# Performance work log

Measured on AMD Instinct MI355X. Metric: run time of the kernel, lower is better.

## Reference

```python
import jax, jax.numpy as jnp
import numpy as np

EPS = 1e-5

def _layer_norm(x, gamma, beta):
    mu = jnp.mean(x, axis=-1, keepdims=True)
    var = jnp.var(x, axis=-1, keepdims=True)
    return (x - mu) * jax.lax.rsqrt(var + EPS) * gamma + beta

def setup_inputs() -> dict:
    key = jax.random.key(0)
    ks = jax.random.split(key, 4)
    B, T, D, H = 16, 2048, 1024, 1024
    s_in = 1.0 / np.sqrt(D)
    return {
        "x": jax.random.normal(ks[0], (B, T, D), dtype=jnp.float32),
        "c": jnp.zeros((B, H), dtype=jnp.float32),
        "W_lt": jax.random.uniform(ks[1], (H, D), jnp.float32, -s_in, s_in),
        "W_g": jax.random.uniform(ks[2], (2 * H, D), jnp.float32, -s_in, s_in),
        "b_g": jnp.zeros((2 * H,), dtype=jnp.float32),
        "gamma_g": jnp.ones((2 * H,), dtype=jnp.float32),
        "beta_g": jnp.zeros((2 * H,), dtype=jnp.float32),
        "gamma_a": jnp.ones((H,), dtype=jnp.float32),
        "beta_a": jnp.zeros((H,), dtype=jnp.float32),
    }

def reference(x, c, W_lt, W_g, b_g, gamma_g, beta_g, gamma_a, beta_a):
    H = W_lt.shape[0]
    # x: [B,T,D]
    x_tilde = jnp.einsum("btd,hd->bth", x, W_lt)            # [B,T,H]
    gate = jax.nn.sigmoid(_layer_norm(jnp.einsum("btd,gd->btg", x, W_g) + b_g, gamma_g, beta_g))
    f = gate[:, :, :H]                                        # forget gate [B,T,H]
    r = gate[:, :, H:]                                        # reset gate  [B,T,H]
    new_data = (1.0 - f) * x_tilde

    def step(c_prev, ft_nd):
        f_t, nd_t = ft_nd
        c_t = f_t * c_prev + nd_t
        return c_t, c_t

    # scan over time: move T to leading axis
    c_final, all_c = jax.lax.scan(step, c, (jnp.swapaxes(f, 0, 1), jnp.swapaxes(new_data, 0, 1)))
    all_c = jnp.swapaxes(all_c, 0, 1)                         # [B,T,H]
    h = r * jax.nn.sigmoid(_layer_norm(all_c, gamma_a, beta_a)) + (1.0 - r) * x
    return (h, c_final)
```

## Files before the change

kernel.cpp:

```cpp
#include <hip/hip_runtime.h>
#include <stdint.h>

typedef unsigned short u16;
typedef u16 us8 __attribute__((ext_vector_type(8)));
typedef uint32_t u32x8 __attribute__((ext_vector_type(8)));
typedef __bf16 bf16x8 __attribute__((ext_vector_type(8)));
typedef float f32x4 __attribute__((ext_vector_type(4)));

#define BB 16
#define TT 2048
#define HH 1024
#define MM 32768
#define NN 3072
#define KK 1024

__device__ __forceinline__ float b2f(u16 u) {
    union { uint32_t i; float f; } v; v.i = ((uint32_t)u) << 16; return v.f;
}
__device__ __forceinline__ u16 f2b(float f) {
    union { uint32_t i; float f; } v; v.f = f;
    uint32_t r = v.i + 0x7fffu + ((v.i >> 16) & 1u);
    return (u16)(r >> 16);
}
__device__ __forceinline__ float sigm(float z) {
    return 1.f / (1.f + __expf(-z));
}
__device__ __forceinline__ void load_lds16(const u16* g, u16* l) {
    __builtin_amdgcn_global_load_lds(
        (const __attribute__((address_space(1))) void*)g,
        (__attribute__((address_space(3))) void*)l, 16, 0, 0);
}

__global__ __launch_bounds__(256) void k_cvt(const float* __restrict__ x,
                                             const float* __restrict__ wlt,
                                             const float* __restrict__ wg,
                                             u16* __restrict__ xb,
                                             u16* __restrict__ wb) {
    long i = (long)(blockIdx.x * 256 + threadIdx.x) * 8;
    const float* s;
    u16* o;
    if (i < 33554432L) { s = x + i; o = xb + i; }
    else {
        long j = i - 33554432L;
        s = (j < 1048576L) ? (wlt + j) : (wg + (j - 1048576L));
        o = wb + j;
    }
    float4 a = *(const float4*)(s);
    float4 b = *(const float4*)(s + 4);
    us8 r;
    r[0] = f2b(a.x); r[1] = f2b(a.y); r[2] = f2b(a.z); r[3] = f2b(a.w);
    r[4] = f2b(b.x); r[5] = f2b(b.y); r[6] = f2b(b.z); r[7] = f2b(b.w);
    *(us8*)o = r;
}

__global__ __launch_bounds__(256) void k_gemm(const u16* __restrict__ A,
                                              const u16* __restrict__ W,
                                              u16* __restrict__ Y) {
    __shared__ u16 As[128 * 32];
    __shared__ u16 Bs[128 * 32];
    const int tid = threadIdx.x;
    const int lane = tid & 63;
    const int q = lane >> 4;
    const int l16 = lane & 15;
    const int w = tid >> 6;
    const int wm = (w >> 1) * 64, wn = (w & 1) * 64;
    const int bx = blockIdx.x, by = blockIdx.y;

    const int s0 = w * 128 + lane;
    const int s1 = w * 128 + 64 + lane;
    const u16* ag0 = A + (size_t)(by * 128 + (s0 >> 2)) * KK + (s0 & 3) * 8;
    const u16* ag1 = A + (size_t)(by * 128 + (s1 >> 2)) * KK + (s1 & 3) * 8;
    const u16* wg0 = W + (size_t)(bx * 128 + (s0 >> 2)) * KK + (s0 & 3) * 8;
    const u16* wg1 = W + (size_t)(bx * 128 + (s1 >> 2)) * KK + (s1 & 3) * 8;
    u16* al0 = As + w * 1024;
    u16* al1 = As + w * 1024 + 512;
    u16* bl0 = Bs + w * 1024;
    u16* bl1 = Bs + w * 1024 + 512;

    f32x4 zero = {0.f, 0.f, 0.f, 0.f};
    f32x4 acc[4][4];
#pragma unroll
    for (int i = 0; i < 4; i++)
#pragma unroll
        for (int j = 0; j < 4; j++) acc[i][j] = zero;

    for (int k0 = 0; k0 < KK; k0 += 32) {
        __syncthreads();
        load_lds16(ag0 + k0, al0);
        load_lds16(ag1 + k0, al1);
        load_lds16(wg0 + k0, bl0);
        load_lds16(wg1 + k0, bl1);
        __syncthreads();
        bf16x8 af[4], bv[4];
#pragma unroll
        for (int i = 0; i < 4; i++)
            af[i] = *(const bf16x8*)&As[(wm + i * 16 + l16) * 32 + q * 8];
#pragma unroll
        for (int j = 0; j < 4; j++)
            bv[j] = *(const bf16x8*)&Bs[(wn + j * 16 + l16) * 32 + q * 8];
#pragma unroll
        for (int i = 0; i < 4; i++)
#pragma unroll
            for (int j = 0; j < 4; j++)
                acc[i][j] = __builtin_amdgcn_mfma_f32_16x16x32_bf16(
                    af[i], bv[j], acc[i][j], 0, 0, 0);
    }

#pragma unroll
    for (int i = 0; i < 4; i++) {
#pragma unroll
        for (int rg = 0; rg < 4; rg++) {
            int row = by * 128 + wm + i * 16 + q * 4 + rg;
            u16* yp = Y + (size_t)row * NN + bx * 128 + wn + l16;
#pragma unroll
            for (int j = 0; j < 4; j++) yp[j * 16] = f2b(acc[i][j][rg]);
        }
    }
}

__global__ __launch_bounds__(256) void k_lnsig(const u16* __restrict__ Y,
                                               const float* __restrict__ bg,
                                               const float* __restrict__ gg,
                                               const float* __restrict__ bt,
                                               uint32_t* __restrict__ FN,
                                               u16* __restrict__ R) {
    const int row = blockIdx.x;
    const int t = threadIdx.x;
    const u16* yr = Y + (size_t)row * 3072;
    us8 gv = *(const us8*)(yr + 1024 + t * 8);
    float z[8];
    float s = 0.f, s2 = 0.f;
#pragma unroll
    for (int k = 0; k < 8; k++) {
        z[k] = b2f(gv[k]) + bg[t * 8 + k];
        s += z[k];
        s2 += z[k] * z[k];
    }
#pragma unroll
    for (int m = 1; m < 64; m <<= 1) {
        s += __shfl_xor(s, m);
        s2 += __shfl_xor(s2, m);
    }
    __shared__ float red[8];
    if ((t & 63) == 0) { red[t >> 6] = s; red[(t >> 6) + 4] = s2; }
    __syncthreads();
    s = red[0] + red[1] + red[2] + red[3];
    s2 = red[4] + red[5] + red[6] + red[7];
    const float mu = s * (1.f / 2048.f);
    const float inv = rsqrtf(s2 * (1.f / 2048.f) - mu * mu + 1e-5f);
    float gate[8];
#pragma unroll
    for (int k = 0; k < 8; k++)
        gate[k] = sigm((z[k] - mu) * inv * gg[t * 8 + k] + bt[t * 8 + k]);
    if (t < 128) {
        us8 xt = *(const us8*)(yr + t * 8);
        u32x8 fn;
#pragma unroll
        for (int k = 0; k < 8; k++) {
            u16 fb = f2b(gate[k]);
            u16 nb = f2b((1.f - gate[k]) * b2f(xt[k]));
            fn[k] = (uint32_t)fb | ((uint32_t)nb << 16);
        }
        *(u32x8*)(FN + (size_t)row * 1024 + t * 8) = fn;
    } else {
        us8 ro;
#pragma unroll
        for (int k = 0; k < 8; k++) ro[k] = f2b(gate[k]);
        *(us8*)(R + (size_t)row * 1024 + (t - 128) * 8) = ro;
    }
}

__global__ __launch_bounds__(256) void k_scan1(const uint32_t* __restrict__ FN,
                                               float2* __restrict__ agg) {
    int u = blockIdx.x * 256 + threadIdx.x;
    int h = u & 1023;
    int chunk = (u >> 10) & 31;
    int b = u >> 15;
    int base = (b * 2048 + chunk * 64) * 1024 + h;
    float Fp = 1.f, Np = 0.f;
#pragma unroll 4
    for (int i = 0; i < 64; i++) {
        uint32_t v = FN[base + i * 1024];
        float f = b2f((u16)(v & 0xffffu));
        float n = b2f((u16)(v >> 16));
        Np = fmaf(f, Np, n);
        Fp *= f;
    }
    agg[(b * 1024 + h) * 32 + chunk] = make_float2(Fp, Np);
}

__global__ __launch_bounds__(256) void k_scan2(const float2* __restrict__ agg,
                                               const float* __restrict__ c0,
                                               float* __restrict__ P) {
    int u = blockIdx.x * 256 + threadIdx.x;
    float c = c0[u];
    const float2* a = agg + (size_t)u * 32;
    float* p = P + (size_t)u * 32;
#pragma unroll 4
    for (int k = 0; k < 32; k++) {
        p[k] = c;
        float2 fn = a[k];
        c = fmaf(fn.x, c, fn.y);
    }
}

__global__ __launch_bounds__(256) void k_scan3(const uint32_t* __restrict__ FN,
                                               const float* __restrict__ P,
                                               u16* __restrict__ C,
                                               float* __restrict__ cfin) {
    int u = blockIdx.x * 256 + threadIdx.x;
    int h = u & 1023;
    int chunk = (u >> 10) & 31;
    int b = u >> 15;
    int base = (b * 2048 + chunk * 64) * 1024 + h;
    float c = P[(b * 1024 + h) * 32 + chunk];
#pragma unroll 4
    for (int i = 0; i < 64; i++) {
        uint32_t v = FN[base + i * 1024];
        float f = b2f((u16)(v & 0xffffu));
        float n = b2f((u16)(v >> 16));
        c = fmaf(f, c, n);
        C[base + i * 1024] = f2b(c);
    }
    if (chunk == 31) cfin[b * 1024 + h] = c;
}

__global__ __launch_bounds__(256) void k_final(const u16* __restrict__ C,
                                               const u16* __restrict__ R,
                                               const u16* __restrict__ xb,
                                               const float* __restrict__ ga,
                                               const float* __restrict__ ba,
                                               float* __restrict__ Ho) {
    const int w = threadIdx.x >> 6, lane = threadIdx.x & 63;
    const int row = blockIdx.x * 4 + w;
    const int col = lane * 16;
    const u16* cp = C + (size_t)row * 1024 + col;
    us8 cv0 = *(const us8*)cp;
    us8 cv1 = *(const us8*)(cp + 8);
    float c[16];
    float s = 0.f, s2 = 0.f;
#pragma unroll
    for (int k = 0; k < 8; k++) { c[k] = b2f(cv0[k]); c[8 + k] = b2f(cv1[k]); }
#pragma unroll
    for (int k = 0; k < 16; k++) { s += c[k]; s2 += c[k] * c[k]; }
#pragma unroll
    for (int m = 1; m < 64; m <<= 1) {
        s += __shfl_xor(s, m);
        s2 += __shfl_xor(s2, m);
    }
    const float mu = s * (1.f / 1024.f);
    const float inv = rsqrtf(s2 * (1.f / 1024.f) - mu * mu + 1e-5f);
    const u16* rp = R + (size_t)row * 1024 + col;
    us8 rv0 = *(const us8*)rp;
    us8 rv1 = *(const us8*)(rp + 8);
    const u16* xp = xb + (size_t)row * 1024 + col;
    us8 xv0 = *(const us8*)xp;
    us8 xv1 = *(const us8*)(xp + 8);
    float ho[16];
#pragma unroll
    for (int k = 0; k < 16; k++) {
        float sg = sigm((c[k] - mu) * inv * ga[col + k] + ba[col + k]);
        float rr = b2f(k < 8 ? rv0[k] : rv1[k - 8]);
        float xx = b2f(k < 8 ? xv0[k] : xv1[k - 8]);
        ho[k] = rr * sg + (1.f - rr) * xx;
    }
    float* op = Ho + (size_t)row * 1024 + col;
    *(float4*)(op)      = *(float4*)&ho[0];
    *(float4*)(op + 4)  = *(float4*)&ho[4];
    *(float4*)(op + 8)  = *(float4*)&ho[8];
    *(float4*)(op + 12) = *(float4*)&ho[12];
}

extern "C" void kernel_launch(void* const* d_in, const int* in_sizes, int n_in,
                              void* d_out, int out_size, void* d_ws, size_t ws_size,
                              hipStream_t stream) {
    const float* x   = (const float*)d_in[0];
    const float* c0  = (const float*)d_in[1];
    const float* wlt = (const float*)d_in[2];
    const float* wg  = (const float*)d_in[3];
    const float* bg  = (const float*)d_in[4];
    const float* gg  = (const float*)d_in[5];
    const float* btg = (const float*)d_in[6];
    const float* ga  = (const float*)d_in[7];
    const float* ba  = (const float*)d_in[8];
    float* out = (float*)d_out;

    char* ws = (char*)d_ws;
    u16* xb      = (u16*)(ws);
    u16* wb      = (u16*)(ws + 67108864);
    u16* y       = (u16*)(ws + 73400320);
    uint32_t* FN = (uint32_t*)(ws + 274726912);
    u16* R       = (u16*)(ws + 408944640);
    float2* agg  = (float2*)(ws + 476053504);
    float* P     = (float*)(ws + 480247808);
    u16* C       = y;

    k_cvt<<<17920, 256, 0, stream>>>(x, wlt, wg, xb, wb);
    k_gemm<<<dim3(24, 256), 256, 0, stream>>>(xb, wb, y);
    k_lnsig<<<32768, 256, 0, stream>>>(y, bg, gg, btg, FN, R);
    k_scan1<<<2048, 256, 0, stream>>>(FN, agg);
    k_scan2<<<64, 256, 0, stream>>>(agg, c0, P);
    k_scan3<<<2048, 256, 0, stream>>>(FN, P, C, out + (size_t)33554432);
    k_final<<<8192, 256, 0, stream>>>(C, R, xb, ga, ba, out);
}
```

Before: 712.4 us.

## Fuse scan pass 3 with final layernorm-sigmoid output and vectorize scan loads

Merges the third scan pass and the final output kernel into one kernel. Each 512-thread block owns a full 1024-wide row for a 64-step chunk, so the per-timestep layernorm over H is computed in-block with a shuffle and shared-memory reduction, and the bf16 C buffer is never written or read back. The scan kernels now handle two h values per thread with 8-byte loads, and the agg/P layout is changed to be h-contiguous for coalesced access. The cost is a __syncthreads per timestep, only 512 blocks in flight, and a serial dependency through the chunk.

```diff
diff --git a/kernel.cpp b/kernel.cpp
--- a/kernel.cpp
+++ b/kernel.cpp
@@ -173,102 +173,86 @@
 __global__ __launch_bounds__(256) void k_scan1(const uint32_t* __restrict__ FN,
                                                float2* __restrict__ agg) {
     int u = blockIdx.x * 256 + threadIdx.x;
-    int h = u & 1023;
-    int chunk = (u >> 10) & 31;
-    int b = u >> 15;
-    int base = (b * 2048 + chunk * 64) * 1024 + h;
-    float Fp = 1.f, Np = 0.f;
+    int h2 = u & 511;
+    int chunk = (u >> 9) & 31;
+    int b = u >> 14;
+    size_t base = (size_t)(b * 2048 + chunk * 64) * 1024 + h2 * 2;
+    float F0 = 1.f, N0 = 0.f, F1 = 1.f, N1 = 0.f;
 #pragma unroll 4
     for (int i = 0; i < 64; i++) {
-        uint32_t v = FN[base + i * 1024];
-        float f = b2f((u16)(v & 0xffffu));
-        float n = b2f((u16)(v >> 16));
-        Np = fmaf(f, Np, n);
-        Fp *= f;
-    }
-    agg[(b * 1024 + h) * 32 + chunk] = make_float2(Fp, Np);
+        uint2 v = *(const uint2*)(FN + base + (size_t)i * 1024);
+        float f0 = b2f((u16)(v.x & 0xffffu)), n0 = b2f((u16)(v.x >> 16));
+        float f1 = b2f((u16)(v.y & 0xffffu)), n1 = b2f((u16)(v.y >> 16));
+        N0 = fmaf(f0, N0, n0); F0 *= f0;
+        N1 = fmaf(f1, N1, n1); F1 *= f1;
+    }
+    float4 o = {F0, N0, F1, N1};
+    *(float4*)&agg[(size_t)(b * 32 + chunk) * 1024 + h2 * 2] = o;
 }
 
 __global__ __launch_bounds__(256) void k_scan2(const float2* __restrict__ agg,
                                                const float* __restrict__ c0,
                                                float* __restrict__ P) {
     int u = blockIdx.x * 256 + threadIdx.x;
+    int b = u >> 10, h = u & 1023;
     float c = c0[u];
-    const float2* a = agg + (size_t)u * 32;
-    float* p = P + (size_t)u * 32;
 #pragma unroll 4
     for (int k = 0; k < 32; k++) {
-        p[k] = c;
-        float2 fn = a[k];
+        size_t idx = (size_t)(b * 32 + k) * 1024 + h;
+        P[idx] = c;
+        float2 fn = agg[idx];
         c = fmaf(fn.x, c, fn.y);
     }
 }
 
-__global__ __launch_bounds__(256) void k_scan3(const uint32_t* __restrict__ FN,
-                                               const float* __restrict__ P,
-                                               u16* __restrict__ C,
-                                               float* __restrict__ cfin) {
-    int u = blockIdx.x * 256 + threadIdx.x;
-    int h = u & 1023;
-    int chunk = (u >> 10) & 31;
-    int b = u >> 15;
-    int base = (b * 2048 + chunk * 64) * 1024 + h;
-    float c = P[(b * 1024 + h) * 32 + chunk];
-#pragma unroll 4
+__global__ __launch_bounds__(512) void k_scanout(const uint32_t* __restrict__ FN,
+                                                 const float* __restrict__ P,
+                                                 const u16* __restrict__ R,
+                                                 const u16* __restrict__ xb,
+                                                 const float* __restrict__ ga,
+                                                 const float* __restrict__ ba,
+                                                 float* __restrict__ out,
+                                                 float* __restrict__ cfin) {
+    __shared__ float2 red[2][8];
+    const int t = threadIdx.x;
+    const int b = blockIdx.x >> 5, chunk = blockIdx.x & 31;
+    const int h = t * 2;
+    const int w = t >> 6, lane = t & 63;
+    float2 cp = *(const float2*)&P[(size_t)(b * 32 + chunk) * 1024 + h];
+    float c0 = cp.x, c1 = cp.y;
+    const float g0 = ga[h], g1 = ga[h + 1];
+    const float be0 = ba[h], be1 = ba[h + 1];
+    const size_t base = (size_t)(b * 2048 + chunk * 64) * 1024 + h;
+#pragma unroll 2
     for (int i = 0; i < 64; i++) {
-        uint32_t v = FN[base + i * 1024];
-        float f = b2f((u16)(v & 0xffffu));
-        float n = b2f((u16)(v >> 16));
-        c = fmaf(f, c, n);
-        C[base + i * 1024] = f2b(c);
-    }
-    if (chunk == 31) cfin[b * 1024 + h] = c;
-}
-
-__global__ __launch_bounds__(256) void k_final(const u16* __restrict__ C,
-                                               const u16* __restrict__ R,
-                                               const u16* __restrict__ xb,
-                                               const float* __restrict__ ga,
-                                               const float* __restrict__ ba,
-                                               float* __restrict__ Ho) {
-    const int w = threadIdx.x >> 6, lane = threadIdx.x & 63;
-    const int row = blockIdx.x * 4 + w;
-    const int col = lane * 16;
-    const u16* cp = C + (size_t)row * 1024 + col;
-    us8 cv0 = *(const us8*)cp;
-    us8 cv1 = *(const us8*)(cp + 8);
-    float c[16];
-    float s = 0.f, s2 = 0.f;
-#pragma unroll
-    for (int k = 0; k < 8; k++) { c[k] = b2f(cv0[k]); c[8 + k] = b2f(cv1[k]); }
-#pragma unroll
-    for (int k = 0; k < 16; k++) { s += c[k]; s2 += c[k] * c[k]; }
-#pragma unroll
-    for (int m = 1; m < 64; m <<= 1) {
-        s += __shfl_xor(s, m);
-        s2 += __shfl_xor(s2, m);
-    }
-    const float mu = s * (1.f / 1024.f);
-    const float inv = rsqrtf(s2 * (1.f / 1024.f) - mu * mu + 1e-5f);
-    const u16* rp = R + (size_t)row * 1024 + col;
-    us8 rv0 = *(const us8*)rp;
-    us8 rv1 = *(const us8*)(rp + 8);
-    const u16* xp = xb + (size_t)row * 1024 + col;
-    us8 xv0 = *(const us8*)xp;
-    us8 xv1 = *(const us8*)(xp + 8);
-    float ho[16];
-#pragma unroll
-    for (int k = 0; k < 16; k++) {
-        float sg = sigm((c[k] - mu) * inv * ga[col + k] + ba[col + k]);
-        float rr = b2f(k < 8 ? rv0[k] : rv1[k - 8]);
-        float xx = b2f(k < 8 ? xv0[k] : xv1[k - 8]);
-        ho[k] = rr * sg + (1.f - rr) * xx;
-    }
-    float* op = Ho + (size_t)row * 1024 + col;
-    *(float4*)(op)      = *(float4*)&ho[0];
-    *(float4*)(op + 4)  = *(float4*)&ho[4];
-    *(float4*)(op + 8)  = *(float4*)&ho[8];
-    *(float4*)(op + 12) = *(float4*)&ho[12];
+        const size_t ro = base + (size_t)i * 1024;
+        uint2 fn = *(const uint2*)(FN + ro);
+        uint32_t rv = *(const uint32_t*)(R + ro);
+        uint32_t xv = *(const uint32_t*)(xb + ro);
+        c0 = fmaf(b2f((u16)(fn.x & 0xffffu)), c0, b2f((u16)(fn.x >> 16)));
+        c1 = fmaf(b2f((u16)(fn.y & 0xffffu)), c1, b2f((u16)(fn.y >> 16)));
+        float s = c0 + c1, s2 = c0 * c0 + c1 * c1;
+#pragma unroll
+        for (int m = 1; m < 64; m <<= 1) {
+            s += __shfl_xor(s, m);
+            s2 += __shfl_xor(s2, m);
+        }
+        const int p = i & 1;
+        if (lane == 0) red[p][w] = make_float2(s, s2);
+        __syncthreads();
+        s = 0.f; s2 = 0.f;
+#pragma unroll
+        for (int k = 0; k < 8; k++) { float2 v = red[p][k]; s += v.x; s2 += v.y; }
+        const float mu = s * (1.f / 1024.f);
+        const float inv = rsqrtf(s2 * (1.f / 1024.f) - mu * mu + 1e-5f);
+        const float sg0 = sigm((c0 - mu) * inv * g0 + be0);
+        const float sg1 = sigm((c1 - mu) * inv * g1 + be1);
+        const float r0 = b2f((u16)(rv & 0xffffu)), r1 = b2f((u16)(rv >> 16));
+        const float x0 = b2f((u16)(xv & 0xffffu)), x1 = b2f((u16)(xv >> 16));
+        float2 ho = {r0 * sg0 + (1.f - r0) * x0, r1 * sg1 + (1.f - r1) * x1};
+        *(float2*)(out + ro) = ho;
+    }
+    if (chunk == 31) *(float2*)(cfin + b * 1024 + h) = make_float2(c0, c1);
 }
 
 extern "C" void kernel_launch(void* const* d_in, const int* in_sizes, int n_in,
@@ -293,13 +277,12 @@
     u16* R       = (u16*)(ws + 408944640);
     float2* agg  = (float2*)(ws + 476053504);
     float* P     = (float*)(ws + 480247808);
-    u16* C       = y;
 
     k_cvt<<<17920, 256, 0, stream>>>(x, wlt, wg, xb, wb);
     k_gemm<<<dim3(24, 256), 256, 0, stream>>>(xb, wb, y);
     k_lnsig<<<32768, 256, 0, stream>>>(y, bg, gg, btg, FN, R);
-    k_scan1<<<2048, 256, 0, stream>>>(FN, agg);
+    k_scan1<<<1024, 256, 0, stream>>>(FN, agg);
     k_scan2<<<64, 256, 0, stream>>>(agg, c0, P);
-    k_scan3<<<2048, 256, 0, stream>>>(FN, P, C, out + (size_t)33554432);
-    k_final<<<8192, 256, 0, stream>>>(C, R, xb, ga, ba, out);
-}
+    k_scanout<<<512, 512, 0, stream>>>(FN, P, R, xb, ga, ba, out,
+                                       out + (size_t)33554432);
+}
```

Result: faster. 691.5 us (-2.9%).
